# Performance work log

Hardware: AMD Instinct MI355X
Metric: run time of the kernel (lower is better)

The kernel has to match this reference:

```python
import jax, jax.numpy as jnp
import numpy as np

B, S, D_IN, D_OUT, H = 2, 2048, 1024, 1024, 16
HD = D_OUT // H


def setup_inputs() -> dict:
    key = jax.random.key(0)
    ks = jax.random.split(key, 6)
    s = 0.02
    return {
        "X": jax.random.normal(ks[0], (B, S, D_IN), dtype=jnp.float32),
        "Wq": jax.random.normal(ks[1], (D_OUT, D_IN), dtype=jnp.float32) * s,
        "Wk": jax.random.normal(ks[2], (D_OUT, D_IN), dtype=jnp.float32) * s,
        "Wv": jax.random.normal(ks[3], (D_OUT, D_IN), dtype=jnp.float32) * s,
        "Wo": jax.random.normal(ks[4], (D_OUT, D_OUT), dtype=jnp.float32) * s,
        "bo": jax.random.normal(ks[5], (D_OUT,), dtype=jnp.float32) * s,
    }


def reference(X, Wq, Wk, Wv, Wo, bo):
    b, n, _ = X.shape
    # torch Linear: y = x @ W^T
    Q = (X @ Wq.T).reshape(b, n, H, HD).transpose(0, 2, 1, 3)  # [b,h,s,hd]
    K = (X @ Wk.T).reshape(b, n, H, HD).transpose(0, 2, 1, 3)
    V = (X @ Wv.T).reshape(b, n, H, HD).transpose(0, 2, 1, 3)
    S_ = jnp.einsum('bhqd,bhkd->bhqk', Q, K)  # [b,h,s,s]
    causal = jnp.triu(jnp.ones((n, n), dtype=bool), k=1)
    S_ = jnp.where(causal, -jnp.inf, S_)
    W = jax.nn.softmax(S_ / jnp.sqrt(jnp.float32(HD)), axis=-1)
    Z = jnp.einsum('bhqk,bhkd->bhqd', W, V)
    Z = Z.transpose(0, 2, 1, 3).reshape(b, n, D_OUT)
    return Z @ Wo.T + bo
```

## Files before the change

### kernel.cpp

```cpp
#include <hip/hip_runtime.h>
#include <stdint.h>

typedef __bf16 bf16x8 __attribute__((ext_vector_type(8)));
typedef float  f32x4  __attribute__((ext_vector_type(4)));

#define S_   2048
#define DM   1024
#define QSCALE 0.18033688011112042f

__device__ __forceinline__ unsigned short f2b(float f) {
    uint32_t u = __builtin_bit_cast(uint32_t, f);
    u += 0x7fffu + ((u >> 16) & 1u);
    return (unsigned short)(u >> 16);
}

__device__ __forceinline__ uint32_t pack2bf(float a, float b) {
    uint32_t ua = __builtin_bit_cast(uint32_t, a) + 0x8000u;
    uint32_t ub = __builtin_bit_cast(uint32_t, b) + 0x8000u;
    return __builtin_amdgcn_perm(ub, ua, 0x07060302);
}

__device__ __forceinline__ void glds16(const void* g, void* l) {
    __builtin_amdgcn_global_load_lds(
        (const __attribute__((address_space(1))) void*)g,
        (__attribute__((address_space(3))) void*)l, 16, 0, 0);
}

__global__ void cvt_all(const float* __restrict__ X,
                        const float* __restrict__ Wq, const float* __restrict__ Wk,
                        const float* __restrict__ Wv,
                        unsigned short* __restrict__ Xb, unsigned short* __restrict__ Wb)
{
    size_t i = ((size_t)blockIdx.x * 256 + threadIdx.x) * 4;
    const float* src;
    unsigned short* dst;
    size_t off;
    if (i < (size_t)4194304) { src = X; dst = Xb; off = i; }
    else {
        size_t j = i - 4194304;
        int sel = (int)(j >> 20);
        off = j & 1048575;
        src = (sel == 0) ? Wq : (sel == 1) ? Wk : Wv;
        dst = Wb + (size_t)sel * 1048576;
    }
    float4 v = *(const float4*)&src[off];
    uint2 o;
    o.x = pack2bf(v.x, v.y);
    o.y = pack2bf(v.z, v.w);
    *(uint2*)&dst[off] = o;
}

__global__ void cvt_wo(const float* __restrict__ Wo, unsigned short* __restrict__ Wob)
{
    size_t i = ((size_t)blockIdx.x * 256 + threadIdx.x) * 4;
    float4 v = *(const float4*)&Wo[i];
    uint2 o;
    o.x = pack2bf(v.x, v.y);
    o.y = pack2bf(v.z, v.w);
    *(uint2*)&Wob[i] = o;
}

__global__ __launch_bounds__(256, 2)
void qkv_gemm(const unsigned short* __restrict__ Xb,
              const unsigned short* __restrict__ Wqb,
              const unsigned short* __restrict__ Wkb,
              const unsigned short* __restrict__ Wvb,
              unsigned short* __restrict__ Qo, unsigned short* __restrict__ Ko,
              unsigned short* __restrict__ Vto)
{
    __shared__ unsigned short Ash[128 * 32];
    __shared__ unsigned short Bsh[128 * 32];

    const int t = threadIdx.x;
    const int lane = t & 63, w = t >> 6;
    const int lcol = lane & 15, quad = lane >> 4;
    const int z = blockIdx.z;
    const int rowBase = ((z == 2) ? blockIdx.x : blockIdx.y) * 128;
    const int colBase = ((z == 2) ? blockIdx.y : blockIdx.x) * 128;
    const unsigned short* aPtr = (z == 2) ? Wvb : Xb;
    const unsigned short* bPtr = (z == 0) ? Wqb : (z == 1) ? Wkb : Xb;
    const int wr = (w >> 1) * 64, wc = (w & 1) * 64;

    f32x4 acc[4][4];
    #pragma unroll
    for (int i = 0; i < 4; ++i)
        #pragma unroll
        for (int j = 0; j < 4; ++j) acc[i][j] = (f32x4){0.f,0.f,0.f,0.f};

    for (int k0 = 0; k0 < DM; k0 += 32) {
        __syncthreads();
        #pragma unroll
        for (int p = 0; p < 2; ++p) {
            int ci = p * 256 + t;
            glds16(&aPtr[(size_t)(rowBase + (ci >> 2)) * DM + k0 + (ci & 3) * 8], &Ash[ci * 8]);
        }
        #pragma unroll
        for (int p = 0; p < 2; ++p) {
            int ci = p * 256 + t;
            glds16(&bPtr[(size_t)(colBase + (ci >> 2)) * DM + k0 + (ci & 3) * 8], &Bsh[ci * 8]);
        }
        __syncthreads();
        bf16x8 af[4], bfr[4];
        #pragma unroll
        for (int i = 0; i < 4; ++i) af[i]  = *(const bf16x8*)&Ash[(wr + i*16 + lcol)*32 + quad*8];
        #pragma unroll
        for (int i = 0; i < 4; ++i) bfr[i] = *(const bf16x8*)&Bsh[(wc + i*16 + lcol)*32 + quad*8];
        #pragma unroll
        for (int i = 0; i < 4; ++i)
            #pragma unroll
            for (int j = 0; j < 4; ++j)
                acc[i][j] = __builtin_amdgcn_mfma_f32_16x16x32_bf16(af[i], bfr[j], acc[i][j], 0, 0, 0);
    }

    unsigned short* Cm = (z == 0) ? Qo : (z == 1) ? Ko : Vto;
    const int ld = (z == 2) ? (S_ * 2) : DM;
    const float sc = (z == 0) ? QSCALE : 1.0f;
    #pragma unroll
    for (int i = 0; i < 4; ++i)
        #pragma unroll
        for (int j = 0; j < 4; ++j)
            #pragma unroll
            for (int r = 0; r < 4; ++r) {
                int row = rowBase + wr + i*16 + quad*4 + r;
                int col = colBase + wc + j*16 + lcol;
                Cm[(size_t)row * ld + col] = f2b(acc[i][j][r] * sc);
            }
}

__global__ __launch_bounds__(512, 4)
void attn_kernel(const unsigned short* __restrict__ Q,
                 const unsigned short* __restrict__ K,
                 const unsigned short* __restrict__ Vt,
                 unsigned short* __restrict__ Z)
{
    __shared__ unsigned short Ks[128 * 72];
    __shared__ unsigned short Vts[64 * 136];
    __shared__ unsigned short Ps[128 * 136];

    const int t = threadIdx.x;
    const int lane = t & 63, w = t >> 6;
    const int lcol = lane & 15, quad = lane >> 4;

    const int g = blockIdx.x;
    const int xcd = g & 7, slot = g >> 3;
    const int bh = xcd * 4 + (slot & 3);
    const int raw = slot >> 2;
    const int tile = (raw < 8) ? (15 - 2 * raw) : (2 * (raw - 8));
    const int b = bh >> 4, h = bh & 15;
    const int q0 = tile * 128;
    const int nchunk = tile + 1;

    const unsigned short* Qg = Q + (size_t)(b * S_ + q0) * DM + h * 64;
    const unsigned short* Kg = K + (size_t)(b * S_) * DM + h * 64;
    const unsigned short* Vg = Vt + (size_t)(h * 64) * (S_ * 2) + b * S_;

    bf16x8 qf[2];
    #pragma unroll
    for (int kd = 0; kd < 2; ++kd)
        qf[kd] = *(const bf16x8*)&Qg[(size_t)(w*16 + lcol) * DM + kd*32 + quad*8];

    bool mk[4];
    #pragma unroll
    for (int r = 0; r < 4; ++r) mk[r] = (quad*4 + r) > lcol;

    float lpart = 0.f;
    f32x4 o[4];
    #pragma unroll
    for (int nd = 0; nd < 4; ++nd) o[nd] = (f32x4){0.f,0.f,0.f,0.f};

    const int kr = t >> 3, kch = t & 7;
    const int vr = t >> 4, vch = t & 15;

    uint4 kreg[2], vreg[2];
    kreg[0] = *(const uint4*)&Kg[(size_t)(kr)      * DM + kch * 8];
    kreg[1] = *(const uint4*)&Kg[(size_t)(64 + kr) * DM + kch * 8];
    vreg[0] = *(const uint4*)&Vg[(size_t)(vr)      * (S_ * 2) + vch * 8];
    vreg[1] = *(const uint4*)&Vg[(size_t)(32 + vr) * (S_ * 2) + vch * 8];

    for (int c = 0; c < nchunk; ++c) {
        __syncthreads();
        *(uint4*)&Ks[(kr)      * 72 + kch * 8] = kreg[0];
        *(uint4*)&Ks[(64 + kr) * 72 + kch * 8] = kreg[1];
        *(uint4*)&Vts[(vr)      * 136 + vch * 8] = vreg[0];
        *(uint4*)&Vts[(32 + vr) * 136 + vch * 8] = vreg[1];
        if (c + 1 < nchunk) {
            const int kn = (c + 1) * 128;
            kreg[0] = *(const uint4*)&Kg[(size_t)(kn + kr)      * DM + kch * 8];
            kreg[1] = *(const uint4*)&Kg[(size_t)(kn + 64 + kr) * DM + kch * 8];
            vreg[0] = *(const uint4*)&Vg[(size_t)(vr)      * (S_ * 2) + kn + vch * 8];
            vreg[1] = *(const uint4*)&Vg[(size_t)(32 + vr) * (S_ * 2) + kn + vch * 8];
        }
        __syncthreads();

        const bool diag = (c == nchunk - 1);
        const int nkmax = diag ? (w + 1) : 8;
        const int kdmax = diag ? ((w >> 1) + 1) : 4;

        #pragma unroll
        for (int nk = 0; nk < 8; ++nk) {
            if (nk < nkmax) {
                f32x4 s = (f32x4){0.f,0.f,0.f,0.f};
                bf16x8 ak0 = *(const bf16x8*)&Ks[(nk*16 + lcol)*72 + quad*8];
                s = __builtin_amdgcn_mfma_f32_16x16x32_bf16(ak0, qf[0], s, 0, 0, 0);
                bf16x8 ak1 = *(const bf16x8*)&Ks[(nk*16 + lcol)*72 + 32 + quad*8];
                s = __builtin_amdgcn_mfma_f32_16x16x32_bf16(ak1, qf[1], s, 0, 0, 0);
                float p0 = __builtin_amdgcn_exp2f(s[0]);
                float p1 = __builtin_amdgcn_exp2f(s[1]);
                float p2 = __builtin_amdgcn_exp2f(s[2]);
                float p3 = __builtin_amdgcn_exp2f(s[3]);
                if (diag && nk == w) {
                    p0 = mk[0] ? 0.f : p0;
                    p1 = mk[1] ? 0.f : p1;
                    p2 = mk[2] ? 0.f : p2;
                    p3 = mk[3] ? 0.f : p3;
                }
                lpart += (p0 + p1) + (p2 + p3);
                uint2 pk;
                pk.x = pack2bf(p0, p1);
                pk.y = pack2bf(p2, p3);
                *(uint2*)&Ps[(w*16 + lcol) * 136 + nk*16 + quad*4] = pk;
            } else if (nk < 2*kdmax) {
                *(uint2*)&Ps[(w*16 + lcol) * 136 + nk*16 + quad*4] = (uint2){0u, 0u};
            }
        }

        #pragma unroll
        for (int kd2 = 0; kd2 < 4; ++kd2) {
            if (kd2 < kdmax) {
                bf16x8 ap = *(const bf16x8*)&Ps[(w*16 + lcol) * 136 + kd2*32 + quad*8];
                #pragma unroll
                for (int nd = 0; nd < 4; ++nd) {
                    bf16x8 bv = *(const bf16x8*)&Vts[(nd*16 + lcol) * 136 + kd2*32 + quad*8];
                    o[nd] = __builtin_amdgcn_mfma_f32_16x16x32_bf16(ap, bv, o[nd], 0, 0, 0);
                }
            }
        }
    }

    lpart += __shfl_xor(lpart, 16);
    lpart += __shfl_xor(lpart, 32);
    float linv = 1.0f / lpart;
    #pragma unroll
    for (int r = 0; r < 4; ++r) {
        float lr = __shfl(linv, quad*4 + r);
        unsigned short* Zr = Z + (size_t)(b*S_ + q0 + w*16 + quad*4 + r) * DM + h*64;
        #pragma unroll
        for (int nd = 0; nd < 4; ++nd)
            Zr[nd*16 + lcol] = f2b(o[nd][r] * lr);
    }
}

__global__ __launch_bounds__(512, 2)
void out_gemm(const unsigned short* __restrict__ A,
              const unsigned short* __restrict__ Wob, const float* __restrict__ bo,
              float* __restrict__ Out)
{
    __shared__ unsigned short Ash[128 * 32];
    __shared__ unsigned short Bsh[128 * 32];

    const int t = threadIdx.x;
    const int lane = t & 63, w = t >> 6;
    const int lcol = lane & 15, quad = lane >> 4;
    const int rowBase = blockIdx.y * 128;
    const int colBase = blockIdx.x * 128;
    const int wr = (w >> 2) * 64, wc = (w & 3) * 32;

    f32x4 acc[4][2];
    #pragma unroll
    for (int i = 0; i < 4; ++i)
        #pragma unroll
        for (int j = 0; j < 2; ++j) acc[i][j] = (f32x4){0.f,0.f,0.f,0.f};

    for (int k0 = 0; k0 < DM; k0 += 32) {
        __syncthreads();
        glds16(&A[(size_t)(rowBase + (t >> 2)) * DM + k0 + (t & 3) * 8], &Ash[t * 8]);
        glds16(&Wob[(size_t)(colBase + (t >> 2)) * DM + k0 + (t & 3) * 8], &Bsh[t * 8]);
        __syncthreads();
        bf16x8 af[4], bfr[2];
        #pragma unroll
        for (int i = 0; i < 4; ++i) af[i]  = *(const bf16x8*)&Ash[(wr + i*16 + lcol)*32 + quad*8];
        #pragma unroll
        for (int j = 0; j < 2; ++j) bfr[j] = *(const bf16x8*)&Bsh[(wc + j*16 + lcol)*32 + quad*8];
        #pragma unroll
        for (int i = 0; i < 4; ++i)
            #pragma unroll
            for (int j = 0; j < 2; ++j)
                acc[i][j] = __builtin_amdgcn_mfma_f32_16x16x32_bf16(af[i], bfr[j], acc[i][j], 0, 0, 0);
    }

    float bb[2];
    #pragma unroll
    for (int j = 0; j < 2; ++j) bb[j] = bo[colBase + wc + j*16 + lcol];

    #pragma unroll
    for (int i = 0; i < 4; ++i)
        #pragma unroll
        for (int j = 0; j < 2; ++j)
            #pragma unroll
            for (int r = 0; r < 4; ++r) {
                int row = rowBase + wr + i*16 + quad*4 + r;
                int col = colBase + wc + j*16 + lcol;
                Out[(size_t)row * DM + col] = acc[i][j][r] + bb[j];
            }
}

extern "C" void kernel_launch(void* const* d_in, const int* in_sizes, int n_in,
                              void* d_out, int out_size, void* d_ws, size_t ws_size,
                              hipStream_t stream) {
    const float* X  = (const float*)d_in[0];
    const float* Wq = (const float*)d_in[1];
    const float* Wk = (const float*)d_in[2];
    const float* Wv = (const float*)d_in[3];
    const float* Wo = (const float*)d_in[4];
    const float* bo = (const float*)d_in[5];
    float* out = (float*)d_out;

    unsigned short* Xb  = (unsigned short*)d_ws;
    unsigned short* Qw  = Xb + (size_t)4096 * 1024;
    unsigned short* Kw  = Qw + (size_t)4096 * 1024;
    unsigned short* Vtw = Kw + (size_t)4096 * 1024;
    unsigned short* Zb  = Xb;
    unsigned short* Wob = Qw;
    unsigned short* Wb  = (unsigned short*)d_out;

    cvt_all<<<dim3(7168), 256, 0, stream>>>(X, Wq, Wk, Wv, Xb, Wb);
    qkv_gemm<<<dim3(8, 32, 3), 256, 0, stream>>>(Xb, Wb, Wb + (size_t)1048576,
                                                 Wb + (size_t)2097152, Qw, Kw, Vtw);
    attn_kernel<<<dim3(512), 512, 0, stream>>>(Qw, Kw, Vtw, Zb);
    cvt_wo<<<dim3(1024), 256, 0, stream>>>(Wo, Wob);
    out_gemm<<<dim3(8, 32), 512, 0, stream>>>(Zb, Wob, bo, out);
}
```

Before: 205.2 us.

## Shrink attention K/V chunks to 64, drop register prefetch, retile output GEMM

The attention kernel now streams 64-key chunks instead of 128, which shrinks shared memory so more blocks can be resident (launch bounds raised to 8). It also drops the register double-buffered prefetch in favour of a direct load-then-sync, and replaces the XCD-aware block swizzle with a plain 2D grid. The output GEMM moves to 256-thread blocks with 64x128 tiles, doubling the block count. The aims are higher occupancy and better CU fill, but the change adds twice as many barriers per key range and gives up latency hiding from the prefetch and L2 locality from the swizzle.

After: 185.2 us. 9.7% less time.

```diff
diff --git a/kernel.cpp b/kernel.cpp
--- a/kernel.cpp
+++ b/kernel.cpp
@@ -127,28 +127,26 @@
             }
 }
 
-__global__ __launch_bounds__(512, 4)
+__global__ __launch_bounds__(512, 8)
 void attn_kernel(const unsigned short* __restrict__ Q,
                  const unsigned short* __restrict__ K,
                  const unsigned short* __restrict__ Vt,
                  unsigned short* __restrict__ Z)
 {
-    __shared__ unsigned short Ks[128 * 72];
-    __shared__ unsigned short Vts[64 * 136];
-    __shared__ unsigned short Ps[128 * 136];
+    __shared__ unsigned short Ks[64 * 72];
+    __shared__ unsigned short Vts[64 * 72];
+    __shared__ unsigned short Ps[128 * 72];
 
     const int t = threadIdx.x;
     const int lane = t & 63, w = t >> 6;
     const int lcol = lane & 15, quad = lane >> 4;
 
-    const int g = blockIdx.x;
-    const int xcd = g & 7, slot = g >> 3;
-    const int bh = xcd * 4 + (slot & 3);
-    const int raw = slot >> 2;
-    const int tile = (raw < 8) ? (15 - 2 * raw) : (2 * (raw - 8));
+    const int bh = blockIdx.x;
     const int b = bh >> 4, h = bh & 15;
+    const int y = blockIdx.y;
+    const int tile = (y < 8) ? (15 - y) : (y - 8);
     const int q0 = tile * 128;
-    const int nchunk = tile + 1;
+    const int nchunk = 2 * tile + 2;
 
     const unsigned short* Qg = Q + (size_t)(b * S_ + q0) * DM + h * 64;
     const unsigned short* Kg = K + (size_t)(b * S_) * DM + h * 64;
@@ -168,36 +166,23 @@
     #pragma unroll
     for (int nd = 0; nd < 4; ++nd) o[nd] = (f32x4){0.f,0.f,0.f,0.f};
 
-    const int kr = t >> 3, kch = t & 7;
-    const int vr = t >> 4, vch = t & 15;
-
-    uint4 kreg[2], vreg[2];
-    kreg[0] = *(const uint4*)&Kg[(size_t)(kr)      * DM + kch * 8];
-    kreg[1] = *(const uint4*)&Kg[(size_t)(64 + kr) * DM + kch * 8];
-    vreg[0] = *(const uint4*)&Vg[(size_t)(vr)      * (S_ * 2) + vch * 8];
-    vreg[1] = *(const uint4*)&Vg[(size_t)(32 + vr) * (S_ * 2) + vch * 8];
+    const int sr = t >> 3, sch = t & 7;
 
     for (int c = 0; c < nchunk; ++c) {
-        __syncthreads();
-        *(uint4*)&Ks[(kr)      * 72 + kch * 8] = kreg[0];
-        *(uint4*)&Ks[(64 + kr) * 72 + kch * 8] = kreg[1];
-        *(uint4*)&Vts[(vr)      * 136 + vch * 8] = vreg[0];
-        *(uint4*)&Vts[(32 + vr) * 136 + vch * 8] = vreg[1];
-        if (c + 1 < nchunk) {
-            const int kn = (c + 1) * 128;
-            kreg[0] = *(const uint4*)&Kg[(size_t)(kn + kr)      * DM + kch * 8];
-            kreg[1] = *(const uint4*)&Kg[(size_t)(kn + 64 + kr) * DM + kch * 8];
-            vreg[0] = *(const uint4*)&Vg[(size_t)(vr)      * (S_ * 2) + kn + vch * 8];
-            vreg[1] = *(const uint4*)&Vg[(size_t)(32 + vr) * (S_ * 2) + kn + vch * 8];
-        }
-        __syncthreads();
-
-        const bool diag = (c == nchunk - 1);
-        const int nkmax = diag ? (w + 1) : 8;
-        const int kdmax = diag ? ((w >> 1) + 1) : 4;
-
-        #pragma unroll
-        for (int nk = 0; nk < 8; ++nk) {
+        const int kc = c * 64;
+        __syncthreads();
+        *(uint4*)&Ks[sr * 72 + sch * 8] =
+            *(const uint4*)&Kg[(size_t)(kc + sr) * DM + sch * 8];
+        *(uint4*)&Vts[sr * 72 + sch * 8] =
+            *(const uint4*)&Vg[(size_t)sr * (S_ * 2) + kc + sch * 8];
+        __syncthreads();
+
+        const int m = tile * 8 + w - c * 4;
+        const int nkmax = (m >= 3) ? 4 : (m + 1);
+        const int kdmax = (nkmax + 1) >> 1;
+
+        #pragma unroll
+        for (int nk = 0; nk < 4; ++nk) {
             if (nk < nkmax) {
                 f32x4 s = (f32x4){0.f,0.f,0.f,0.f};
                 bf16x8 ak0 = *(const bf16x8*)&Ks[(nk*16 + lcol)*72 + quad*8];
@@ -208,7 +193,7 @@
                 float p1 = __builtin_amdgcn_exp2f(s[1]);
                 float p2 = __builtin_amdgcn_exp2f(s[2]);
                 float p3 = __builtin_amdgcn_exp2f(s[3]);
-                if (diag && nk == w) {
+                if (nk == m) {
                     p0 = mk[0] ? 0.f : p0;
                     p1 = mk[1] ? 0.f : p1;
                     p2 = mk[2] ? 0.f : p2;
@@ -218,19 +203,19 @@
                 uint2 pk;
                 pk.x = pack2bf(p0, p1);
                 pk.y = pack2bf(p2, p3);
-                *(uint2*)&Ps[(w*16 + lcol) * 136 + nk*16 + quad*4] = pk;
+                *(uint2*)&Ps[(w*16 + lcol) * 72 + nk*16 + quad*4] = pk;
             } else if (nk < 2*kdmax) {
-                *(uint2*)&Ps[(w*16 + lcol) * 136 + nk*16 + quad*4] = (uint2){0u, 0u};
+                *(uint2*)&Ps[(w*16 + lcol) * 72 + nk*16 + quad*4] = (uint2){0u, 0u};
             }
         }
 
         #pragma unroll
-        for (int kd2 = 0; kd2 < 4; ++kd2) {
+        for (int kd2 = 0; kd2 < 2; ++kd2) {
             if (kd2 < kdmax) {
-                bf16x8 ap = *(const bf16x8*)&Ps[(w*16 + lcol) * 136 + kd2*32 + quad*8];
+                bf16x8 ap = *(const bf16x8*)&Ps[(w*16 + lcol) * 72 + kd2*32 + quad*8];
                 #pragma unroll
                 for (int nd = 0; nd < 4; ++nd) {
-                    bf16x8 bv = *(const bf16x8*)&Vts[(nd*16 + lcol) * 136 + kd2*32 + quad*8];
+                    bf16x8 bv = *(const bf16x8*)&Vts[(nd*16 + lcol) * 72 + kd2*32 + quad*8];
                     o[nd] = __builtin_amdgcn_mfma_f32_16x16x32_bf16(ap, bv, o[nd], 0, 0, 0);
                 }
             }
@@ -250,52 +235,56 @@
     }
 }
 
-__global__ __launch_bounds__(512, 2)
+__global__ __launch_bounds__(256, 4)
 void out_gemm(const unsigned short* __restrict__ A,
               const unsigned short* __restrict__ Wob, const float* __restrict__ bo,
               float* __restrict__ Out)
 {
-    __shared__ unsigned short Ash[128 * 32];
+    __shared__ unsigned short Ash[64 * 32];
     __shared__ unsigned short Bsh[128 * 32];
 
     const int t = threadIdx.x;
     const int lane = t & 63, w = t >> 6;
     const int lcol = lane & 15, quad = lane >> 4;
-    const int rowBase = blockIdx.y * 128;
+    const int rowBase = blockIdx.y * 64;
     const int colBase = blockIdx.x * 128;
-    const int wr = (w >> 2) * 64, wc = (w & 3) * 32;
-
-    f32x4 acc[4][2];
-    #pragma unroll
-    for (int i = 0; i < 4; ++i)
-        #pragma unroll
-        for (int j = 0; j < 2; ++j) acc[i][j] = (f32x4){0.f,0.f,0.f,0.f};
+    const int wr = (w >> 1) * 32, wc = (w & 1) * 64;
+
+    f32x4 acc[2][4];
+    #pragma unroll
+    for (int i = 0; i < 2; ++i)
+        #pragma unroll
+        for (int j = 0; j < 4; ++j) acc[i][j] = (f32x4){0.f,0.f,0.f,0.f};
 
     for (int k0 = 0; k0 < DM; k0 += 32) {
         __syncthreads();
         glds16(&A[(size_t)(rowBase + (t >> 2)) * DM + k0 + (t & 3) * 8], &Ash[t * 8]);
-        glds16(&Wob[(size_t)(colBase + (t >> 2)) * DM + k0 + (t & 3) * 8], &Bsh[t * 8]);
-        __syncthreads();
-        bf16x8 af[4], bfr[2];
-        #pragma unroll
-        for (int i = 0; i < 4; ++i) af[i]  = *(const bf16x8*)&Ash[(wr + i*16 + lcol)*32 + quad*8];
-        #pragma unroll
-        for (int j = 0; j < 2; ++j) bfr[j] = *(const bf16x8*)&Bsh[(wc + j*16 + lcol)*32 + quad*8];
-        #pragma unroll
-        for (int i = 0; i < 4; ++i)
+        #pragma unroll
+        for (int p = 0; p < 2; ++p) {
+            int ci = p * 256 + t;
+            glds16(&Wob[(size_t)(colBase + (ci >> 2)) * DM + k0 + (ci & 3) * 8], &Bsh[ci * 8]);
+        }
+        __syncthreads();
+        bf16x8 af[2], bfr[4];
+        #pragma unroll
+        for (int i = 0; i < 2; ++i) af[i]  = *(const bf16x8*)&Ash[(wr + i*16 + lcol)*32 + quad*8];
+        #pragma unroll
+        for (int j = 0; j < 4; ++j) bfr[j] = *(const bf16x8*)&Bsh[(wc + j*16 + lcol)*32 + quad*8];
+        #pragma unroll
+        for (int i = 0; i < 2; ++i)
             #pragma unroll
-            for (int j = 0; j < 2; ++j)
+            for (int j = 0; j < 4; ++j)
                 acc[i][j] = __builtin_amdgcn_mfma_f32_16x16x32_bf16(af[i], bfr[j], acc[i][j], 0, 0, 0);
     }
 
-    float bb[2];
-    #pragma unroll
-    for (int j = 0; j < 2; ++j) bb[j] = bo[colBase + wc + j*16 + lcol];
-
-    #pragma unroll
-    for (int i = 0; i < 4; ++i)
-        #pragma unroll
-        for (int j = 0; j < 2; ++j)
+    float bb[4];
+    #pragma unroll
+    for (int j = 0; j < 4; ++j) bb[j] = bo[colBase + wc + j*16 + lcol];
+
+    #pragma unroll
+    for (int i = 0; i < 2; ++i)
+        #pragma unroll
+        for (int j = 0; j < 4; ++j)
             #pragma unroll
             for (int r = 0; r < 4; ++r) {
                 int row = rowBase + wr + i*16 + quad*4 + r;
@@ -326,7 +315,7 @@
     cvt_all<<<dim3(7168), 256, 0, stream>>>(X, Wq, Wk, Wv, Xb, Wb);
     qkv_gemm<<<dim3(8, 32, 3), 256, 0, stream>>>(Xb, Wb, Wb + (size_t)1048576,
                                                  Wb + (size_t)2097152, Qw, Kw, Vtw);
-    attn_kernel<<<dim3(512), 512, 0, stream>>>(Qw, Kw, Vtw, Zb);
+    attn_kernel<<<dim3(32, 16), 512, 0, stream>>>(Qw, Kw, Vtw, Zb);
     cvt_wo<<<dim3(1024), 256, 0, stream>>>(Wo, Wob);
-    out_gemm<<<dim3(8, 32), 512, 0, stream>>>(Zb, Wob, bo, out);
-}
+    out_gemm<<<dim3(8, 64), 256, 0, stream>>>(Zb, Wob, bo, out);
+}
```
